# Performance work log

Hardware: AMD Instinct MI355X
Metric: run time of the kernel (lower is better)

The kernel has to match this reference:

```python
import jax, jax.numpy as jnp
import numpy as np

N_NODES = 50000
N_EDGES = 400000
IN_DIM = 4
HID = 32
NCLASSES = 4
N_ITERS = 3


def setup_inputs() -> dict:
    key = jax.random.key(0)
    ks = jax.random.split(key, 8)

    def w(k, shape, fan_in):
        return (jax.random.normal(k, shape, dtype=jnp.float32) / np.sqrt(fan_in)).astype(jnp.float32)

    x = jax.random.normal(ks[0], (3, N_NODES, IN_DIM), dtype=jnp.float32)
    edge_index = jax.random.randint(ks[1], (3, 2, N_EDGES), 0, N_NODES, dtype=jnp.int64)
    hi = HID + IN_DIM  # 36: feats of m = cat([H, X])
    return {
        "x": x,
        "edge_index": edge_index,
        "in_W": w(ks[2], (3, IN_DIM, HID), IN_DIM),
        "in_b": jnp.zeros((3, HID), jnp.float32),
        "eW1": w(ks[3], (3, 2 * hi, HID), 2 * hi),
        "eb1": jnp.zeros((3, HID), jnp.float32),
        "eW2": w(ks[4], (3, HID, 1), HID),
        "eb2": jnp.zeros((3, 1), jnp.float32),
        "nW1": w(ks[5], (3, 3 * hi, HID), 3 * hi),
        "nb1": jnp.zeros((3, HID), jnp.float32),
        "nW2": w(ks[6], (3, HID, HID), HID),
        "nb2": jnp.zeros((3, HID), jnp.float32),
    }


def _forward(x, edge_index, in_W, in_b, eW1, eb1, eW2, eb2, nW1, nb1, nW2, nb2):
    n_nodes = x.shape[1]

    def edge_net(j, m, row, col):
        # B: [E, C, 2*(h+in)] -- detached in the original module
        B = jax.lax.stop_gradient(jnp.concatenate([m[col], m[row]], axis=-1))
        t = jnp.tanh(B @ eW1[j] + eb1[j])
        t = jnp.tanh(t @ eW2[j] + eb2[j])  # [E, C, 1]
        return jax.nn.softmax(t, axis=1)  # softmax over class dim

    def node_net(j, m, ea, row, col):
        mi = jax.ops.segment_sum(ea * m[row], col, num_segments=n_nodes)
        mo = jax.ops.segment_sum(ea * m[col], row, num_segments=n_nodes)
        M = jnp.concatenate([mi, mo, m], axis=-1)  # [N, C, 3*(h+in)]
        t = jnp.tanh(M @ nW1[j] + nb1[j])
        return jnp.tanh(t @ nW2[j] + nb2[j])  # [N, C, hid]

    rows = [edge_index[j, 0] for j in range(3)]
    cols = [edge_index[j, 1] for j in range(3)]
    # X: node feats repeated per class, [N, C, in]
    X = [jnp.broadcast_to(x[j][:, None, :], (n_nodes, NCLASSES, x.shape[-1])) for j in range(3)]
    H = [jnp.tanh(X[j] @ in_W[j] + in_b[j]) for j in range(3)]
    m = [jnp.concatenate([H[j], X[j]], axis=-1) for j in range(3)]

    for _ in range(N_ITERS):
        for j in range(3):
            ea = edge_net(j, m[j], rows[j], cols[j])
            H[j] = node_net(j, m[j], ea, rows[j], cols[j])
        m = [jnp.concatenate([H[j], X[j]], axis=-1) for j in range(3)]

    # classify_node=False: final edge-network pass per plane, squeeze -> [E, C]
    ret = [edge_net(j, m[j], rows[j], cols[j])[..., 0] for j in range(3)]
    return jnp.concatenate(ret, axis=0)  # [3*E, C]


def reference(x, edge_index, in_W, in_b, eW1, eb1, eW2, eb2, nW1, nb1, nW2, nb2):
    return _forward(x, edge_index, in_W, in_b, eW1, eb1, eW2, eb2, nW1, nb1, nW2, nb2)
```

## Files before the change

### kernel.cpp

```cpp
#include <hip/hip_runtime.h>
#include <hip/hip_fp16.h>

#define N_NODES 50000
#define N_EDGES 400000
#define NCLS 4
#define HID 32
#define HI 36
#define ROWS_P (N_NODES * NCLS)
#define PADCAP 672000
#define SLICES 8
#define BUCKS_PER_SLICE (N_NODES / SLICES)

__device__ __forceinline__ float fast_tanh(float x) {
    float e = __builtin_amdgcn_exp2f(x * 2.885390081777927f);
    float r = __builtin_amdgcn_rcpf(1.0f + e);
    return fmaf(-2.0f, r, 1.0f);
}

#if __has_builtin(__builtin_amdgcn_fdot2)
typedef _Float16 h2v __attribute__((ext_vector_type(2)));
__device__ __forceinline__ float fdot2f(__half2 a, __half2 b, float c) {
    return __builtin_amdgcn_fdot2(__builtin_bit_cast(h2v, a),
                                  __builtin_bit_cast(h2v, b), c, false);
}
#else
__device__ __forceinline__ float fdot2f(__half2 a, __half2 b, float c) {
    float2 af = __half22float2(a), bf = __half22float2(b);
    return c + af.x * bf.x + af.y * bf.y;
}
#endif

union F4H8 { float4 f4; __half2 h2[4]; };
union F2H4 { float2 f2; __half2 h2[2]; };

__global__ void k_init(const float* __restrict__ x, const float* __restrict__ W,
                       const float* __restrict__ b, __half* __restrict__ m) {
    unsigned t = blockIdx.x * 256 + threadIdx.x;
    if (t >= N_NODES * HI) return;
    unsigned idx = t % HI;
    unsigned n   = t / HI;
    float x0 = x[n * 4 + 0], x1 = x[n * 4 + 1];
    float x2 = x[n * 4 + 2], x3 = x[n * 4 + 3];
    float val;
    if (idx < 32) {
        float a = b[idx];
        a += x0 * W[idx] + x1 * W[32 + idx] + x2 * W[64 + idx] + x3 * W[96 + idx];
        val = fast_tanh(a);
    } else {
        val = (idx == 32) ? x0 : (idx == 33) ? x1 : (idx == 34) ? x2 : x3;
    }
    __half hv = __float2half_rn(val);
    __half* dst = m + (size_t)n * (NCLS * HI) + idx;
    dst[0] = hv; dst[HI] = hv; dst[2 * HI] = hv; dst[3 * HI] = hv;
}

__global__ void k_pass1(const int* __restrict__ rowI, const int* __restrict__ colI,
                        int* __restrict__ inCnt, int* __restrict__ outCnt,
                        int* __restrict__ tmpLi) {
    unsigned e = blockIdx.x * 256 + threadIdx.x;
    if (e >= N_EDGES) return;
    int r = rowI[e], cn = colI[e];
    int liIn  = atomicAdd(&inCnt[cn], 1);
    int liOut = atomicAdd(&outCnt[r], 1);
    tmpLi[e] = liIn | (liOut << 16);
}

__global__ void k_scan(const int* __restrict__ inCnt, const int* __restrict__ outCnt,
                       int* __restrict__ inOffRaw, int* __restrict__ pinOff,
                       int* __restrict__ poutOff) {
    const int* cnt = (blockIdx.x == 2) ? outCnt : inCnt;
    int* off = (blockIdx.x == 0) ? inOffRaw : (blockIdx.x == 1) ? pinOff : poutOff;
    bool pad = blockIdx.x != 0;
    __shared__ int sh[16];
    __shared__ int carry;
    int tid = threadIdx.x;
    int lane = tid & 63, wid = tid >> 6;
    if (tid == 0) carry = 0;
    __syncthreads();
    for (int base = 0; base < N_NODES; base += 1024) {
        int i = base + tid;
        int v = (i < N_NODES) ? cnt[i] : 0;
        if (pad) v = (v + 7) & ~7;
        int val = v;
#pragma unroll
        for (int d = 1; d < 64; d <<= 1) {
            int t = __shfl_up(val, d, 64);
            if (lane >= d) val += t;
        }
        if (lane == 63) sh[wid] = val;
        __syncthreads();
        if (tid < 16) {
            int s = sh[tid];
#pragma unroll
            for (int d = 1; d < 16; d <<= 1) {
                int t = __shfl_up(s, d, 16);
                if (tid >= d) s += t;
            }
            sh[tid] = s;
        }
        __syncthreads();
        int waveOff = (wid == 0) ? 0 : sh[wid - 1];
        int incl = val + waveOff + carry;
        if (i < N_NODES) off[i] = incl - v;
        __syncthreads();
        if (tid == 1023) carry = incl;
        __syncthreads();
    }
    if (tid == 0) off[N_NODES] = carry;
}

__global__ void k_pass2(const int* __restrict__ rowI, const int* __restrict__ colI,
                        const int* __restrict__ tmpLi,
                        const int* __restrict__ inOffRaw, const int* __restrict__ pinOff,
                        const int* __restrict__ poutOff,
                        int4* __restrict__ edgeRec,
                        unsigned short* __restrict__ inPrt,
                        unsigned short* __restrict__ outPrt) {
    unsigned b = blockIdx.x;
    unsigned slice = b & (SLICES - 1);
    unsigned e = (b >> 3) * 256 + threadIdx.x;
    if (e >= N_EDGES) return;
    int r = rowI[e], cn = colI[e];
    int li = tmpLi[e];
    int liIn  = li & 0xFFFF;
    int liOut = (int)(((unsigned)li) >> 16);
    unsigned lo = slice * BUCKS_PER_SLICE;
    if ((unsigned)(cn - lo) < BUCKS_PER_SLICE) {
        int dense = inOffRaw[cn] + liIn;
        int piP   = pinOff[cn] + liIn;
        int poP   = poutOff[r] + liOut;
        edgeRec[dense] = make_int4(r | (cn << 16), piP, poP, (int)e);
        inPrt[piP] = (unsigned short)r;
    }
    if ((unsigned)(r - lo) < BUCKS_PER_SLICE) {
        int poP = poutOff[r] + liOut;
        outPrt[poP] = (unsigned short)cn;
    }
}


__global__ void k_gemm5(const __half* __restrict__ m,
                        const float* __restrict__ eW1, const float* __restrict__ nW1,
                        const float* __restrict__ eb1, const float* __restrict__ nb1,
                        __half* __restrict__ u, __half* __restrict__ v,
                        __half* __restrict__ p, __half* __restrict__ q,
                        __half* __restrict__ r) {
    constexpr int RPB = 32;
    __shared__ __half sm[RPB * 40];
    unsigned tid = threadIdx.x;
    unsigned r0  = blockIdx.x * RPB;
    if (tid < RPB * 9) {
        uint2 d = reinterpret_cast<const uint2*>(m + (size_t)r0 * HI)[tid];
        unsigned row = tid / 9, off = tid % 9;
        *reinterpret_cast<uint2*>(sm + row * 40 + off * 4) = d;
    }
    unsigned o = tid % 160, grp = tid / 160;
    unsigned sub = o >> 5, oo = o & 31;
    const float* W = (sub == 0) ? eW1 : (sub == 1) ? eW1 + 36 * 32 :
                     (sub == 2) ? nW1 : (sub == 3) ? nW1 + 36 * 32 : nW1 + 72 * 32;
    __half* dsth   = (sub == 0) ? u : (sub == 1) ? v : (sub == 2) ? p :
                     (sub == 3) ? q : r;
    float bias = (sub == 0) ? eb1[oo] : (sub == 4) ? nb1[oo] : 0.f;
    __half2 wc[18];
#pragma unroll
    for (int t = 0; t < 18; ++t)
        wc[t] = __floats2half2_rn(W[(2 * t) * 32 + oo], W[(2 * t + 1) * 32 + oo]);
    __syncthreads();
#pragma unroll
    for (int i = 0; i < 16; ++i) {
        unsigned rloc = grp * 16 + i;
        const __half* rowp = sm + rloc * 40;
        F4H8 A0, A1, A2, A3; F2H4 A4;
        A0.f4 = *reinterpret_cast<const float4*>(rowp);
        A1.f4 = *reinterpret_cast<const float4*>(rowp + 8);
        A2.f4 = *reinterpret_cast<const float4*>(rowp + 16);
        A3.f4 = *reinterpret_cast<const float4*>(rowp + 24);
        A4.f2 = *reinterpret_cast<const float2*>(rowp + 32);
        float acc = bias;
#pragma unroll
        for (int t = 0; t < 4; ++t) acc = fdot2f(A0.h2[t], wc[t], acc);
#pragma unroll
        for (int t = 0; t < 4; ++t) acc = fdot2f(A1.h2[t], wc[4 + t], acc);
#pragma unroll
        for (int t = 0; t < 4; ++t) acc = fdot2f(A2.h2[t], wc[8 + t], acc);
#pragma unroll
        for (int t = 0; t < 4; ++t) acc = fdot2f(A3.h2[t], wc[12 + t], acc);
        acc = fdot2f(A4.h2[0], wc[16], acc);
        acc = fdot2f(A4.h2[1], wc[17], acc);
        dsth[(size_t)(r0 + rloc) * 32 + oo] = __float2half_rn(acc);
    }
}

__global__ void k_gemm2(const __half* __restrict__ m, const float* __restrict__ W0,
                        const float* __restrict__ W1, const float* __restrict__ eb1,
                        __half* __restrict__ o0, __half* __restrict__ o1) {
    constexpr int RPB = 32;
    __shared__ __half sm[RPB * 40];
    unsigned tid = threadIdx.x;
    unsigned r0  = blockIdx.x * RPB;
    for (unsigned i = tid; i < RPB * 9; i += 256) {
        uint2 d = reinterpret_cast<const uint2*>(m + (size_t)r0 * HI)[i];
        unsigned row = i / 9, off = i % 9;
        *reinterpret_cast<uint2*>(sm + row * 40 + off * 4) = d;
    }
    unsigned o = tid % 64, grp = tid / 64;
    unsigned sub = o >> 5, oo = o & 31;
    const float* W = sub ? W1 : W0;
    __half* dst    = sub ? o1 : o0;
    float bias = sub ? 0.f : eb1[oo];
    __half2 wc[18];
#pragma unroll
    for (int t = 0; t < 18; ++t)
        wc[t] = __floats2half2_rn(W[(2 * t) * 32 + oo], W[(2 * t + 1) * 32 + oo]);
    __syncthreads();
#pragma unroll
    for (int i = 0; i < 8; ++i) {
        unsigned rloc = grp * 8 + i;
        const __half* rowp = sm + rloc * 40;
        F4H8 A0, A1, A2, A3; F2H4 A4;
        A0.f4 = *reinterpret_cast<const float4*>(rowp);
        A1.f4 = *reinterpret_cast<const float4*>(rowp + 8);
        A2.f4 = *reinterpret_cast<const float4*>(rowp + 16);
        A3.f4 = *reinterpret_cast<const float4*>(rowp + 24);
        A4.f2 = *reinterpret_cast<const float2*>(rowp + 32);
        float acc = bias;
#pragma unroll
        for (int t = 0; t < 4; ++t) acc = fdot2f(A0.h2[t], wc[t], acc);
#pragma unroll
        for (int t = 0; t < 4; ++t) acc = fdot2f(A1.h2[t], wc[4 + t], acc);
#pragma unroll
        for (int t = 0; t < 4; ++t) acc = fdot2f(A2.h2[t], wc[8 + t], acc);
#pragma unroll
        for (int t = 0; t < 4; ++t) acc = fdot2f(A3.h2[t], wc[12 + t], acc);
        acc = fdot2f(A4.h2[0], wc[16], acc);
        acc = fdot2f(A4.h2[1], wc[17], acc);
        dst[(size_t)(r0 + rloc) * 32 + oo] = __float2half_rn(acc);
    }
}

template <bool FINAL>
__global__ void k_edge(const int4* __restrict__ edgeRec,
                       const __half* __restrict__ u, const __half* __restrict__ v,
                       const float* __restrict__ w2, const float* __restrict__ b2,
                       __half* __restrict__ eaIn, __half* __restrict__ eaOut,
                       float* __restrict__ dst) {
    unsigned g   = blockIdx.x * 256 + threadIdx.x;
    unsigned c   = g & 3;
    unsigned idx = g >> 2;
    int4 rec = edgeRec[idx];
    unsigned rc  = (unsigned)rec.x;
    unsigned row = rc & 0xFFFFu, col = rc >> 16;
    const float4* u4 = reinterpret_cast<const float4*>(u + (col * 4 + c) * 32);
    const float4* v4 = reinterpret_cast<const float4*>(v + (row * 4 + c) * 32);
    float t2 = b2[0];
#pragma unroll
    for (int i = 0; i < 4; ++i) {
        F4H8 U, V; U.f4 = u4[i]; V.f4 = v4[i];
#pragma unroll
        for (int jj = 0; jj < 4; ++jj) {
            float2 sf = __half22float2(__hadd2(U.h2[jj], V.h2[jj]));
            int o = i * 8 + jj * 2;
            t2 += fast_tanh(sf.x) * w2[o];
            t2 += fast_tanh(sf.y) * w2[o + 1];
        }
    }
    float s  = fast_tanh(t2);
    float m1 = fmaxf(s, __shfl_xor(s, 1, 4));
    float mx = fmaxf(m1, __shfl_xor(m1, 2, 4));
    float ex = __expf(s - mx);
    float sm = ex + __shfl_xor(ex, 1, 4);
    sm = sm + __shfl_xor(sm, 2, 4);
    float val = ex * __builtin_amdgcn_rcpf(sm);
    if (FINAL) {
        dst[(unsigned)rec.w * 4 + c] = val;
    } else {
        __half hv = __float2half_rn(val);
        eaIn[(size_t)c * PADCAP + (unsigned)rec.y] = hv;
        eaOut[(size_t)c * PADCAP + (unsigned)rec.z] = hv;
    }
}

__global__ void __launch_bounds__(64, 4)
k_node(__half* __restrict__ m, const __half* __restrict__ rbuf,
       const __half* __restrict__ p, const __half* __restrict__ q,
       const __half* __restrict__ eaInT, const __half* __restrict__ eaOutT,
       const int* __restrict__ pinOff, const int* __restrict__ poutOff,
       const unsigned short* __restrict__ inPrt,
       const unsigned short* __restrict__ outPrt,
       const float* __restrict__ nW2, const float* __restrict__ nb2) {
    unsigned lane = threadIdx.x;
    unsigned c2 = lane >> 5, k = lane & 31;
    unsigned n = blockIdx.x;
    unsigned gOff0 = c2 * 32 + k;
    unsigned gOff1 = gOff0 + 64;

    float h0 = __half2float(rbuf[((size_t)n * 4 + c2) * 32 + k]);
    float h1 = __half2float(rbuf[((size_t)n * 4 + c2 + 2) * 32 + k]);

    int bi0 = pinOff[n],  biE = pinOff[n + 1];
    int bo0 = poutOff[n], boE = poutOff[n + 1];
    __builtin_assume((bi0 & 7) == 0);
    __builtin_assume((bo0 & 7) == 0);

    const __half* eaI0 = eaInT + (size_t)c2 * PADCAP;
    const __half* eaI1 = eaInT + (size_t)(c2 + 2) * PADCAP;
    const __half* eaO0 = eaOutT + (size_t)c2 * PADCAP;
    const __half* eaO1 = eaOutT + (size_t)(c2 + 2) * PADCAP;

    auto accum = [&](const __half* __restrict__ base, uint4 prtv, uint4 e0v, uint4 e1v) {
        unsigned pr0 = prtv.x & 0xFFFFu, pr1 = prtv.x >> 16;
        unsigned pr2 = prtv.y & 0xFFFFu, pr3 = prtv.y >> 16;
        unsigned pr4 = prtv.z & 0xFFFFu, pr5 = prtv.z >> 16;
        unsigned pr6 = prtv.w & 0xFFFFu, pr7 = prtv.w >> 16;
        __half g0h[8], g1h[8];
        const __half* r0p = base + (size_t)pr0 * 128u; g0h[0] = r0p[gOff0]; g1h[0] = r0p[gOff1];
        const __half* r1p = base + (size_t)pr1 * 128u; g0h[1] = r1p[gOff0]; g1h[1] = r1p[gOff1];
        const __half* r2p = base + (size_t)pr2 * 128u; g0h[2] = r2p[gOff0]; g1h[2] = r2p[gOff1];
        const __half* r3p = base + (size_t)pr3 * 128u; g0h[3] = r3p[gOff0]; g1h[3] = r3p[gOff1];
        const __half* r4p = base + (size_t)pr4 * 128u; g0h[4] = r4p[gOff0]; g1h[4] = r4p[gOff1];
        const __half* r5p = base + (size_t)pr5 * 128u; g0h[5] = r5p[gOff0]; g1h[5] = r5p[gOff1];
        const __half* r6p = base + (size_t)pr6 * 128u; g0h[6] = r6p[gOff0]; g1h[6] = r6p[gOff1];
        const __half* r7p = base + (size_t)pr7 * 128u; g0h[7] = r7p[gOff0]; g1h[7] = r7p[gOff1];
        union { uint4 u4; __half2 h2[4]; } E0, E1;
        E0.u4 = e0v; E1.u4 = e1v;
#pragma unroll
        for (int ii = 0; ii < 4; ++ii) {
            h0 = fdot2f(E0.h2[ii], __halves2half2(g0h[2 * ii], g0h[2 * ii + 1]), h0);
            h1 = fdot2f(E1.h2[ii], __halves2half2(g1h[2 * ii], g1h[2 * ii + 1]), h1);
        }
    };

    uint4 oprt = {0, 0, 0, 0}, oe0 = {0, 0, 0, 0}, oe1 = {0, 0, 0, 0};
    if (bo0 < boE) {
        oprt = *(const uint4*)(outPrt + bo0);
        oe0  = *(const uint4*)(eaO0 + bo0);
        oe1  = *(const uint4*)(eaO1 + bo0);
    }

    if (bi0 < biE) {
        uint4 cprt = *(const uint4*)(inPrt + bi0);
        uint4 ce0  = *(const uint4*)(eaI0 + bi0);
        uint4 ce1  = *(const uint4*)(eaI1 + bi0);
        for (int b = bi0; b < biE; b += 8) {
            uint4 nprt = cprt, ne0 = ce0, ne1 = ce1;
            if (b + 8 < biE) {
                nprt = *(const uint4*)(inPrt + b + 8);
                ne0  = *(const uint4*)(eaI0 + b + 8);
                ne1  = *(const uint4*)(eaI1 + b + 8);
            }
            accum(p, cprt, ce0, ce1);
            cprt = nprt; ce0 = ne0; ce1 = ne1;
        }
    }
    if (bo0 < boE) {
        uint4 cprt = oprt, ce0 = oe0, ce1 = oe1;
        for (int b = bo0; b < boE; b += 8) {
            uint4 nprt = cprt, ne0 = ce0, ne1 = ce1;
            if (b + 8 < boE) {
                nprt = *(const uint4*)(outPrt + b + 8);
                ne0  = *(const uint4*)(eaO0 + b + 8);
                ne1  = *(const uint4*)(eaO1 + b + 8);
            }
            accum(q, cprt, ce0, ce1);
            cprt = nprt; ce0 = ne0; ce1 = ne1;
        }
    }

    float t0 = fast_tanh(h0);
    float t1 = fast_tanh(h1);
    float hh0 = nb2[k], hh1 = hh0;
#pragma unroll
    for (int kk = 0; kk < 32; ++kk) {
        float w = nW2[kk * 32 + k];
        float s0 = __shfl(t0, (int)(c2 * 32 + kk), 64);
        float s1 = __shfl(t1, (int)(c2 * 32 + kk), 64);
        hh0 += s0 * w;
        hh1 += s1 * w;
    }
    m[((size_t)n * 4 + c2) * HI + k]     = __float2half_rn(fast_tanh(hh0));
    m[((size_t)n * 4 + c2 + 2) * HI + k] = __float2half_rn(fast_tanh(hh1));
}

extern "C" void kernel_launch(void* const* d_in, const int* in_sizes, int n_in,
                              void* d_out, int out_size, void* d_ws, size_t ws_size,
                              hipStream_t stream) {
    const float* x   = (const float*)d_in[0];
    const int*   ei  = (const int*)d_in[1];
    const float* inW = (const float*)d_in[2];
    const float* inb = (const float*)d_in[3];
    const float* eW1 = (const float*)d_in[4];
    const float* eb1 = (const float*)d_in[5];
    const float* eW2 = (const float*)d_in[6];
    const float* eb2 = (const float*)d_in[7];
    const float* nW1 = (const float*)d_in[8];
    const float* nb1 = (const float*)d_in[9];
    const float* nW2 = (const float*)d_in[10];
    const float* nb2 = (const float*)d_in[11];
    float* out = (float*)d_out;

    __half* m     = (__half*)d_ws;
    __half* u     = m + (size_t)ROWS_P * HI;
    __half* v     = u + (size_t)ROWS_P * 32;
    __half* p     = v + (size_t)ROWS_P * 32;
    __half* q     = p + (size_t)ROWS_P * 32;
    __half* rbuf  = q + (size_t)ROWS_P * 32;
    __half* eaIn  = rbuf + (size_t)ROWS_P * 32;
    __half* eaOut = eaIn + (size_t)PADCAP * 4;
    unsigned short* inPrt  = (unsigned short*)(eaOut + (size_t)PADCAP * 4);
    unsigned short* outPrt = inPrt + PADCAP;
    int4*   edgeRec = (int4*)(outPrt + PADCAP);
    int*    inOffRaw = (int*)(edgeRec + N_EDGES);
    int*    pinOff   = inOffRaw + (N_NODES + 1);
    int*    poutOff  = pinOff + (N_NODES + 1);
    int*    inCnt    = poutOff + (N_NODES + 1);
    int*    outCnt   = inCnt + N_NODES;
    int*    tmpLi    = (int*)u;

    const int gridE = (N_EDGES + 255) / 256;
    const size_t zeroBytes = (size_t)PADCAP * 4 * 2 * 2 + (size_t)PADCAP * 2 * 2;

    for (int j = 0; j < 3; ++j) {
        const int*   rowI = ei + (size_t)j * 2 * N_EDGES;
        const int*   colI = rowI + N_EDGES;
        const float* eW1j = eW1 + j * 72 * 32;
        const float* eb1j = eb1 + j * 32;
        const float* eW2j = eW2 + j * 32;
        const float* eb2j = eb2 + j;
        const float* nW1j = nW1 + j * 108 * 32;
        const float* nb1j = nb1 + j * 32;
        const float* nW2j = nW2 + j * 1024;
        const float* nb2j = nb2 + j * 32;

        hipMemsetAsync(inCnt, 0, 2 * N_NODES * sizeof(int), stream);
        hipMemsetAsync(eaIn, 0, zeroBytes, stream);
        k_pass1<<<gridE, 256, 0, stream>>>(rowI, colI, inCnt, outCnt, tmpLi);
        k_scan<<<3, 1024, 0, stream>>>(inCnt, outCnt, inOffRaw, pinOff, poutOff);
        k_pass2<<<gridE * SLICES, 256, 0, stream>>>(rowI, colI, tmpLi,
                                                    inOffRaw, pinOff, poutOff,
                                                    edgeRec, inPrt, outPrt);

        k_init<<<(N_NODES * HI + 255) / 256, 256, 0, stream>>>(
            x + (size_t)j * N_NODES * 4, inW + j * 128, inb + j * 32, m);

        for (int it = 0; it < 3; ++it) {
            k_gemm5<<<ROWS_P / 32, 320, 0, stream>>>(m, eW1j, nW1j, eb1j, nb1j,
                                                     u, v, p, q, rbuf);
            k_edge<false><<<N_EDGES * 4 / 256, 256, 0, stream>>>(
                edgeRec, u, v, eW2j, eb2j, eaIn, eaOut, nullptr);
            k_node<<<N_NODES, 64, 0, stream>>>(m, rbuf, p, q, eaIn, eaOut,
                                               pinOff, poutOff, inPrt, outPrt,
                                               nW2j, nb2j);
        }
        k_gemm2<<<ROWS_P / 32, 256, 0, stream>>>(m, eW1j, eW1j + 36 * 32, eb1j, u, v);
        k_edge<true><<<N_EDGES * 4 / 256, 256, 0, stream>>>(
            edgeRec, u, v, eW2j, eb2j, nullptr, nullptr,
            out + (size_t)j * N_EDGES * 4);
    }
}
```

Baseline: 1.591 ms.

## Replace single-block serial prefix scan with three-phase parallel scan

The degree prefix scan ran as three 1024-thread blocks, each looping sequentially over 50000 entries with several barriers per iteration. It is now split into three kernels: per-chunk block sums, a scan of those sums, then a per-chunk local scan plus offset. This spreads the work over many blocks and trades the long serial loop for two extra kernel launches per plane. The code relies on inOffRaw, pinOff and poutOff being contiguous, and on the chunk count (196) fitting in the 256 threads of one block.

```diff
diff --git a/kernel.cpp b/kernel.cpp
--- a/kernel.cpp
+++ b/kernel.cpp
@@ -10,6 +10,7 @@
 #define PADCAP 672000
 #define SLICES 8
 #define BUCKS_PER_SLICE (N_NODES / SLICES)
+#define NCHUNKS ((N_NODES + 255) / 256)
 
 __device__ __forceinline__ float fast_tanh(float x) {
     float e = __builtin_amdgcn_exp2f(x * 2.885390081777927f);
@@ -65,48 +66,65 @@
     tmpLi[e] = liIn | (liOut << 16);
 }
 
-__global__ void k_scan(const int* __restrict__ inCnt, const int* __restrict__ outCnt,
-                       int* __restrict__ inOffRaw, int* __restrict__ pinOff,
-                       int* __restrict__ poutOff) {
-    const int* cnt = (blockIdx.x == 2) ? outCnt : inCnt;
-    int* off = (blockIdx.x == 0) ? inOffRaw : (blockIdx.x == 1) ? pinOff : poutOff;
-    bool pad = blockIdx.x != 0;
-    __shared__ int sh[16];
-    __shared__ int carry;
+__global__ void k_scanA(const int* __restrict__ inCnt, const int* __restrict__ outCnt,
+                        int* __restrict__ bsum) {
+    unsigned v = blockIdx.x / NCHUNKS, chunk = blockIdx.x % NCHUNKS;
+    unsigned i = chunk * 256 + threadIdx.x;
+    const int* cnt = (v == 2) ? outCnt : inCnt;
+    int val = (i < N_NODES) ? cnt[i] : 0;
+    if (v) val = (val + 7) & ~7;
+#pragma unroll
+    for (int d = 1; d < 64; d <<= 1) val += __shfl_xor(val, d, 64);
+    __shared__ int sh[4];
+    unsigned lane = threadIdx.x & 63, wid = threadIdx.x >> 6;
+    if (lane == 0) sh[wid] = val;
+    __syncthreads();
+    if (threadIdx.x == 0) bsum[blockIdx.x] = sh[0] + sh[1] + sh[2] + sh[3];
+}
+
+__global__ void k_scanB(const int* __restrict__ bsum, int* __restrict__ boff,
+                        int* __restrict__ offs) {
+    unsigned v = blockIdx.x;
     int tid = threadIdx.x;
+    int val = (tid < NCHUNKS) ? bsum[v * NCHUNKS + tid] : 0;
     int lane = tid & 63, wid = tid >> 6;
-    if (tid == 0) carry = 0;
+    int incl = val;
+#pragma unroll
+    for (int d = 1; d < 64; d <<= 1) {
+        int t = __shfl_up(incl, d, 64);
+        if (lane >= d) incl += t;
+    }
+    __shared__ int sh[4];
+    if (lane == 63) sh[wid] = incl;
     __syncthreads();
-    for (int base = 0; base < N_NODES; base += 1024) {
-        int i = base + tid;
-        int v = (i < N_NODES) ? cnt[i] : 0;
-        if (pad) v = (v + 7) & ~7;
-        int val = v;
-#pragma unroll
-        for (int d = 1; d < 64; d <<= 1) {
-            int t = __shfl_up(val, d, 64);
-            if (lane >= d) val += t;
-        }
-        if (lane == 63) sh[wid] = val;
-        __syncthreads();
-        if (tid < 16) {
-            int s = sh[tid];
-#pragma unroll
-            for (int d = 1; d < 16; d <<= 1) {
-                int t = __shfl_up(s, d, 16);
-                if (tid >= d) s += t;
-            }
-            sh[tid] = s;
-        }
-        __syncthreads();
-        int waveOff = (wid == 0) ? 0 : sh[wid - 1];
-        int incl = val + waveOff + carry;
-        if (i < N_NODES) off[i] = incl - v;
-        __syncthreads();
-        if (tid == 1023) carry = incl;
-        __syncthreads();
-    }
-    if (tid == 0) off[N_NODES] = carry;
+    int waveOff = (wid == 0) ? 0 : (wid == 1) ? sh[0] :
+                  (wid == 2) ? sh[0] + sh[1] : sh[0] + sh[1] + sh[2];
+    incl += waveOff;
+    if (tid < NCHUNKS) boff[v * NCHUNKS + tid] = incl - val;
+    if (tid == NCHUNKS - 1) offs[(size_t)v * (N_NODES + 1) + N_NODES] = incl;
+}
+
+__global__ void k_scanC(const int* __restrict__ inCnt, const int* __restrict__ outCnt,
+                        const int* __restrict__ boff, int* __restrict__ offs) {
+    unsigned v = blockIdx.x / NCHUNKS, chunk = blockIdx.x % NCHUNKS;
+    unsigned i = chunk * 256 + threadIdx.x;
+    const int* cnt = (v == 2) ? outCnt : inCnt;
+    int val = (i < N_NODES) ? cnt[i] : 0;
+    if (v) val = (val + 7) & ~7;
+    int lane = threadIdx.x & 63, wid = threadIdx.x >> 6;
+    int incl = val;
+#pragma unroll
+    for (int d = 1; d < 64; d <<= 1) {
+        int t = __shfl_up(incl, d, 64);
+        if (lane >= d) incl += t;
+    }
+    __shared__ int sh[4];
+    if (lane == 63) sh[wid] = incl;
+    __syncthreads();
+    int waveOff = (wid == 0) ? 0 : (wid == 1) ? sh[0] :
+                  (wid == 2) ? sh[0] + sh[1] : sh[0] + sh[1] + sh[2];
+    if (i < N_NODES)
+        offs[(size_t)v * (N_NODES + 1) + i] = boff[v * NCHUNKS + chunk] + incl + waveOff - val;
 }
 
 __global__ void k_pass2(const int* __restrict__ rowI, const int* __restrict__ colI,
@@ -414,6 +432,8 @@
     int*    poutOff  = pinOff + (N_NODES + 1);
     int*    inCnt    = poutOff + (N_NODES + 1);
     int*    outCnt   = inCnt + N_NODES;
+    int*    bsum     = outCnt + N_NODES;
+    int*    boff     = bsum + 3 * NCHUNKS;
     int*    tmpLi    = (int*)u;
 
     const int gridE = (N_EDGES + 255) / 256;
@@ -434,7 +454,9 @@
         hipMemsetAsync(inCnt, 0, 2 * N_NODES * sizeof(int), stream);
         hipMemsetAsync(eaIn, 0, zeroBytes, stream);
         k_pass1<<<gridE, 256, 0, stream>>>(rowI, colI, inCnt, outCnt, tmpLi);
-        k_scan<<<3, 1024, 0, stream>>>(inCnt, outCnt, inOffRaw, pinOff, poutOff);
+        k_scanA<<<3 * NCHUNKS, 256, 0, stream>>>(inCnt, outCnt, bsum);
+        k_scanB<<<3, 256, 0, stream>>>(bsum, boff, inOffRaw);
+        k_scanC<<<3 * NCHUNKS, 256, 0, stream>>>(inCnt, outCnt, boff, inOffRaw);
         k_pass2<<<gridE * SLICES, 256, 0, stream>>>(rowI, colI, tmpLi,
                                                     inOffRaw, pinOff, poutOff,
                                                     edgeRec, inPrt, outPrt);
```

Result: faster. 1.473 ms (-7.4%).
